# Optimization experiments

Measured on AMD Instinct MI355X. Metric: run time of the kernel, lower is better.

The kernel has to match this reference:

```python
import jax, jax.numpy as jnp
import numpy as np

N_NODES = 100000
N_EDGES = 1600000
IN_FEATS = 256
N_HEADS = 4
OUT_FEATS = 32
NEG_SLOPE = 0.2


def setup_inputs() -> dict:
    key = jax.random.key(0)
    k0, k1, k2, k3, k4, k5 = jax.random.split(key, 6)
    feat = jax.random.normal(k0, (N_NODES, IN_FEATS), dtype=jnp.float32)
    src = jax.random.randint(k1, (N_EDGES,), 0, N_NODES, dtype=jnp.int32)
    dst = jax.random.randint(k2, (N_EDGES,), 0, N_NODES, dtype=jnp.int32)
    # fc.weight: [num_heads*out_feats, in_feats] (torch Linear layout)
    W = jax.random.normal(k3, (N_HEADS * OUT_FEATS, IN_FEATS), dtype=jnp.float32) * 0.05
    attn_l = jax.random.normal(k4, (1, N_HEADS, OUT_FEATS), dtype=jnp.float32) * 0.1
    attn_r = jax.random.normal(k5, (1, N_HEADS, OUT_FEATS), dtype=jnp.float32) * 0.1
    return {"feat": feat, "src": src, "dst": dst, "W": W, "attn_l": attn_l, "attn_r": attn_r}


def reference(feat, src, dst, W, attn_l, attn_r):
    N = feat.shape[0]
    H, D = attn_l.shape[1], attn_l.shape[2]
    # fc projection -> [N, H, D]
    feat_src = (feat @ W.T).reshape(N, H, D)
    el = jnp.sum(feat_src * attn_l, axis=-1)  # [N, H]
    er = jnp.sum(feat_src * attn_r, axis=-1)  # [N, H]
    # per-edge scores: u_add_v then LeakyReLU  -> [E, H]
    e = jax.nn.leaky_relu(el[src] + er[dst], negative_slope=NEG_SLOPE)
    # edge_softmax: segmented softmax over edges grouped by destination node
    emax = jax.ops.segment_max(e, dst, num_segments=N)  # [N, H]
    emax = jnp.where(jnp.isfinite(emax), emax, jnp.zeros_like(emax))
    ee = jnp.exp(e - emax[dst])  # [E, H]
    denom = jax.ops.segment_sum(ee, dst, num_segments=N)  # [N, H]
    a = ee / denom[dst]  # [E, H]
    # u_mul_e + sum aggregation -> [N, H, D]
    m = feat_src[src] * a[:, :, None]  # [E, H, D]
    rst = jax.ops.segment_sum(m, dst, num_segments=N)
    return rst
```

## Files before the change

kernel.cpp:

```cpp
#include <hip/hip_runtime.h>
#include <hip/hip_bf16.h>
#include <math.h>

#define NN 100000
#define NE 1600000
#define INF_ 256
#define NH 4
#define DH 32
#define NHD 128
#define NEG_SLOPE 0.2f

#define NB3 1563
#define STRIDE 1280
#define EPB 4096
#define NBLK_BIN 391
#define GEMM_BLKS 782
#define SMEM_BYTES 32768

typedef __attribute__((ext_vector_type(8))) short bf16x8;
typedef __attribute__((ext_vector_type(4))) float f32x4;

__device__ __forceinline__ unsigned short f2bf(float f) {
    __hip_bfloat16 b = __float2bfloat16(f);
    return *reinterpret_cast<unsigned short*>(&b);
}

__global__ __launch_bounds__(256) void k_prep0(const float* __restrict__ W,
                                               unsigned short* __restrict__ Wimg,
                                               int* __restrict__ gcur) {
    int t = threadIdx.x;
    int b = blockIdx.x;
    if (b == 16) {
        for (int i = t; i < NB3; i += 256) gcur[i] = 0;
        return;
    }
    int i = b * 256 + t;
    int kt = i >> 9;
    int r = (i >> 2) & 127;
    int g = i & 3;
    int slot = g ^ (r & 7);
    const float* s = &W[(size_t)r * INF_ + kt * 32 + g * 8];
    unsigned short tmp[8];
#pragma unroll
    for (int j = 0; j < 8; j++) tmp[j] = f2bf(s[j]);
    *(bf16x8*)&Wimg[(size_t)kt * 8192 + r * 64 + slot * 8] = *(const bf16x8*)tmp;
}

__global__ __launch_bounds__(256) void k_gemmbin(const float* __restrict__ feat,
                                                 const unsigned short* __restrict__ Wimg,
                                                 const int* __restrict__ src,
                                                 const int* __restrict__ dst,
                                                 const float* __restrict__ al,
                                                 const float* __restrict__ ar,
                                                 unsigned short* __restrict__ fsb,
                                                 float* __restrict__ el,
                                                 float* __restrict__ er,
                                                 int* __restrict__ gcur,
                                                 unsigned* __restrict__ packed) {
    __shared__ __align__(16) char smem[SMEM_BYTES];
    const int t = threadIdx.x;

    if (blockIdx.x >= GEMM_BLKS) {
        int hb = blockIdx.x - GEMM_BLKS;
        int* ldst = (int*)smem;
        int* lc = (int*)(smem + EPB * 4);
        int* wb = (int*)(smem + EPB * 4 + NB3 * 4);
        for (int i = t; i < NB3; i += 256) lc[i] = 0;
        __syncthreads();
        int base = hb * EPB;
#pragma unroll
        for (int j = 0; j < 16; j++) {
            int e = base + j * 256 + t;
            int d = (e < NE) ? dst[e] : -1;
            ldst[j * 256 + t] = d;
            if (d >= 0) atomicAdd(&lc[d >> 6], 1);
        }
        __syncthreads();
        for (int i = t; i < NB3; i += 256) {
            int c = lc[i];
            wb[i] = c ? i * STRIDE + atomicAdd(&gcur[i], c) : 0;
            lc[i] = 0;
        }
        __syncthreads();
#pragma unroll
        for (int j = 0; j < 16; j++) {
            int e = base + j * 256 + t;
            if (e < NE) {
                int d = ldst[j * 256 + t];
                int bk = d >> 6;
                int s = src[e];
                int pos = wb[bk] + atomicAdd(&lc[bk], 1);
                if (pos < (bk + 1) * STRIDE)
                    packed[pos] = ((unsigned)s << 6) | (unsigned)(d & 63);
            }
        }
        return;
    }

    short* sA = (short*)smem;
    short* sB = (short*)(smem + 16384);
    const int brow = blockIdx.x * 128;
    const int wid = t >> 6, lane = t & 63;
    const int wr = wid >> 1, wc = wid & 1;
    const int lg = lane >> 4;
    const int lr = lane & 15;

    f32x4 acc[4][4];
#pragma unroll
    for (int m = 0; m < 4; m++)
#pragma unroll
        for (int n = 0; n < 4; n++) acc[m][n] = (f32x4){0.f, 0.f, 0.f, 0.f};

    const int srow = t >> 1;
    const int cb = (t & 1) * 16;
    const int g0 = cb >> 3;
    const int p0 = (g0 ^ (srow & 7));
    const int p1 = ((g0 + 1) ^ (srow & 7));
    const int grow = brow + srow;
    const bool arow_ok = (grow < NN);
    const char* bimg = (const char*)Wimg;

    float fv[16];
    uint4 wv0, wv1, wv2, wv3;
    if (arow_ok) {
        const float4* pa = (const float4*)&feat[(size_t)grow * INF_ + cb];
        *(float4*)&fv[0] = pa[0];
        *(float4*)&fv[4] = pa[1];
        *(float4*)&fv[8] = pa[2];
        *(float4*)&fv[12] = pa[3];
    } else {
#pragma unroll
        for (int j = 0; j < 16; j++) fv[j] = 0.f;
    }
    wv0 = *(const uint4*)(bimg + t * 16);
    wv1 = *(const uint4*)(bimg + 4096 + t * 16);
    wv2 = *(const uint4*)(bimg + 8192 + t * 16);
    wv3 = *(const uint4*)(bimg + 12288 + t * 16);

    for (int kt = 0; kt < 8; kt++) {
        {
            short sv[16];
#pragma unroll
            for (int j = 0; j < 16; j++) sv[j] = (short)f2bf(fv[j]);
            *(bf16x8*)&sA[srow * 64 + p0 * 8] = *(const bf16x8*)&sv[0];
            *(bf16x8*)&sA[srow * 64 + p1 * 8] = *(const bf16x8*)&sv[8];
            char* bd = (char*)sB;
            *(uint4*)(bd + t * 16) = wv0;
            *(uint4*)(bd + 4096 + t * 16) = wv1;
            *(uint4*)(bd + 8192 + t * 16) = wv2;
            *(uint4*)(bd + 12288 + t * 16) = wv3;
        }
        __syncthreads();
        if (kt < 7) {
            int k0 = (kt + 1) * 32;
            if (arow_ok) {
                const float4* pa = (const float4*)&feat[(size_t)grow * INF_ + k0 + cb];
                *(float4*)&fv[0] = pa[0];
                *(float4*)&fv[4] = pa[1];
                *(float4*)&fv[8] = pa[2];
                *(float4*)&fv[12] = pa[3];
            }
            const char* bsrc = bimg + (size_t)(kt + 1) * 16384;
            wv0 = *(const uint4*)(bsrc + t * 16);
            wv1 = *(const uint4*)(bsrc + 4096 + t * 16);
            wv2 = *(const uint4*)(bsrc + 8192 + t * 16);
            wv3 = *(const uint4*)(bsrc + 12288 + t * 16);
        }
        bf16x8 aF[4], bF[4];
#pragma unroll
        for (int m = 0; m < 4; m++) {
            int r = wr * 64 + m * 16 + lr;
            aF[m] = *(const bf16x8*)&sA[r * 64 + ((lg ^ (r & 7)) * 8)];
        }
#pragma unroll
        for (int n = 0; n < 4; n++) {
            int r = wc * 64 + n * 16 + lr;
            bF[n] = *(const bf16x8*)&sB[r * 64 + ((lg ^ (r & 7)) * 8)];
        }
#pragma unroll
        for (int m = 0; m < 4; m++)
#pragma unroll
            for (int n = 0; n < 4; n++)
                acc[m][n] = __builtin_amdgcn_mfma_f32_16x16x32_bf16(aF[m], bF[n], acc[m][n], 0, 0, 0);
        __syncthreads();
    }
#pragma unroll
    for (int m = 0; m < 4; m++) {
#pragma unroll
        for (int n = 0; n < 4; n++) {
#pragma unroll
            for (int r = 0; r < 4; r++) {
                int gr = brow + wr * 64 + m * 16 + lg * 4 + r;
                if (gr < NN)
                    fsb[(size_t)gr * NHD + wc * 64 + n * 16 + lr] = f2bf(acc[m][n][r]);
            }
        }
    }
    const int hA = wc * 2, hB = wc * 2 + 1;
    const float alA0 = al[hA * 32 + lr], alA1 = al[hA * 32 + 16 + lr];
    const float alB0 = al[hB * 32 + lr], alB1 = al[hB * 32 + 16 + lr];
    const float arA0 = ar[hA * 32 + lr], arA1 = ar[hA * 32 + 16 + lr];
    const float arB0 = ar[hB * 32 + lr], arB1 = ar[hB * 32 + 16 + lr];
#pragma unroll
    for (int m = 0; m < 4; m++) {
#pragma unroll
        for (int r = 0; r < 4; r++) {
            float eA = acc[m][0][r] * alA0 + acc[m][1][r] * alA1;
            float eB = acc[m][2][r] * alB0 + acc[m][3][r] * alB1;
            float fA = acc[m][0][r] * arA0 + acc[m][1][r] * arA1;
            float fB = acc[m][2][r] * arB0 + acc[m][3][r] * arB1;
#pragma unroll
            for (int off = 1; off < 16; off <<= 1) {
                eA += __shfl_xor(eA, off);
                eB += __shfl_xor(eB, off);
                fA += __shfl_xor(fA, off);
                fB += __shfl_xor(fB, off);
            }
            if (lr == 0) {
                int gr = brow + wr * 64 + m * 16 + lg * 4 + r;
                if (gr < NN) {
                    el[gr * 4 + hA] = eA;
                    el[gr * 4 + hB] = eB;
                    er[gr * 4 + hA] = fA;
                    er[gr * 4 + hB] = fB;
                }
            }
        }
    }
}

__global__ __launch_bounds__(256) void k_sortagg(const int* __restrict__ gcur,
                                                 const unsigned* __restrict__ packed,
                                                 const float* __restrict__ el,
                                                 const float* __restrict__ er,
                                                 const uint4* __restrict__ fsb128,
                                                 float* __restrict__ out) {
    __shared__ int lh[64];
    __shared__ int off[65];
    __shared__ int cur[64];
    __shared__ int esrc_l[STRIDE];
    int b = blockIdx.x, t = threadIdx.x;
    int beg = b * STRIDE;
    int cnt = gcur[b];
    if (cnt > STRIDE) cnt = STRIDE;

    if (t < 64) lh[t] = 0;
    __syncthreads();
    for (int k = t; k < cnt; k += 256)
        atomicAdd(&lh[packed[beg + k] & 63u], 1);
    __syncthreads();
    if (t < 64) {
        int v = lh[t];
        int x = v;
#pragma unroll
        for (int o = 1; o < 64; o <<= 1) {
            int y = __shfl_up(x, o);
            if (t >= o) x += y;
        }
        off[t] = x - v;
        cur[t] = x - v;
        if (t == 63) off[64] = x;
    }
    __syncthreads();
    for (int k = t; k < cnt; k += 256) {
        unsigned p = packed[beg + k];
        int pos = atomicAdd(&cur[p & 63u], 1);
        esrc_l[pos] = (int)(p >> 6);
    }
    __syncthreads();

    int lane = t & 63;
    int wv = t >> 6;
    int q = lane >> 4;
    int sl = lane & 15;
    int h = sl >> 2;

#define STEP(eV, vV)                                           \
    {                                                          \
        float sc_ = (eV) + rr;                                 \
        sc_ = sc_ > 0.f ? sc_ : NEG_SLOPE * sc_;               \
        float ee = __expf(sc_);                                \
        den += ee;                                             \
        a0 += ee * __uint_as_float((vV).x << 16);              \
        a1 += ee * __uint_as_float((vV).x & 0xFFFF0000u);      \
        a2 += ee * __uint_as_float((vV).y << 16);              \
        a3 += ee * __uint_as_float((vV).y & 0xFFFF0000u);      \
        a4 += ee * __uint_as_float((vV).z << 16);              \
        a5 += ee * __uint_as_float((vV).z & 0xFFFF0000u);      \
        a6 += ee * __uint_as_float((vV).w << 16);              \
        a7 += ee * __uint_as_float((vV).w & 0xFFFF0000u);      \
    }

    for (int ln = wv * 16; ln < wv * 16 + 16; ln++) {
        int node = (b << 6) + ln;
        if (node >= NN) break;
        int bg = off[ln];
        int en = off[ln + 1];
        float rr = er[node * 4 + h];
        float den = 0.f;
        float a0 = 0.f, a1 = 0.f, a2 = 0.f, a3 = 0.f;
        float a4 = 0.f, a5 = 0.f, a6 = 0.f, a7 = 0.f;
        int k = bg + q;
        for (; k + 4 < en; k += 8) {
            int s0 = esrc_l[k];
            int s1 = esrc_l[k + 4];
            uint4 v0 = fsb128[(size_t)s0 * 16 + sl];
            uint4 v1 = fsb128[(size_t)s1 * 16 + sl];
            float e0 = el[s0 * 4 + h];
            float e1 = el[s1 * 4 + h];
            STEP(e0, v0)
            STEP(e1, v1)
        }
        for (; k < en; k += 4) {
            int s = esrc_l[k];
            uint4 vv = fsb128[(size_t)s * 16 + sl];
            float eV = el[s * 4 + h];
            STEP(eV, vv)
        }
#pragma unroll
        for (int o = 16; o <= 32; o <<= 1) {
            a0 += __shfl_xor(a0, o);
            a1 += __shfl_xor(a1, o);
            a2 += __shfl_xor(a2, o);
            a3 += __shfl_xor(a3, o);
            a4 += __shfl_xor(a4, o);
            a5 += __shfl_xor(a5, o);
            a6 += __shfl_xor(a6, o);
            a7 += __shfl_xor(a7, o);
            den += __shfl_xor(den, o);
        }
        if (q == 0) {
            float inv = den > 0.f ? 1.0f / den : 0.f;
            float4 o0, o1;
            o0.x = a0 * inv; o0.y = a1 * inv; o0.z = a2 * inv; o0.w = a3 * inv;
            o1.x = a4 * inv; o1.y = a5 * inv; o1.z = a6 * inv; o1.w = a7 * inv;
            float* p = &out[(size_t)node * NHD + sl * 8];
            *(float4*)p = o0;
            *(float4*)(p + 4) = o1;
        }
    }
#undef STEP
}

extern "C" void kernel_launch(void* const* d_in, const int* in_sizes, int n_in,
                              void* d_out, int out_size, void* d_ws, size_t ws_size,
                              hipStream_t stream) {
    const float* feat = (const float*)d_in[0];
    const int* src = (const int*)d_in[1];
    const int* dst = (const int*)d_in[2];
    const float* W = (const float*)d_in[3];
    const float* al = (const float*)d_in[4];
    const float* ar = (const float*)d_in[5];
    float* out = (float*)d_out;

    char* ws = (char*)d_ws;
    unsigned short* fsb = (unsigned short*)ws;   ws += (size_t)NN * NHD * 2;
    unsigned* packed = (unsigned*)ws;            ws += (size_t)NB3 * STRIDE * 4;
    float* el = (float*)ws;                      ws += (size_t)NN * NH * 4;
    float* er = (float*)ws;                      ws += (size_t)NN * NH * 4;
    int* gcur = (int*)ws;                        ws += (size_t)NB3 * 4;
    unsigned short* Wimg = (unsigned short*)ws;  ws += (size_t)8 * 8192 * 2;

    k_prep0<<<17, 256, 0, stream>>>(W, Wimg, gcur);
    k_gemmbin<<<GEMM_BLKS + NBLK_BIN, 256, 0, stream>>>(feat, Wimg, src, dst,
                                                        al, ar, fsb, el, er,
                                                        gcur, packed);
    k_sortagg<<<NB3, 256, 0, stream>>>(gcur, packed, el, er,
                                       (const uint4*)fsb, out);
}
```

Measured before the change: 138.5 us.

## Split fused GEMM+binning kernel, enlarge bin chunks, pad global bucket counters

Splits the combined GEMM/edge-binning launch into a separate GEMM kernel and a separate binning kernel. The binning kernel now handles 16384 edges per block (98 blocks instead of 391), which cuts global atomic traffic on the bucket cursors. Those cursors are padded to 64-byte spacing to avoid contention from false sharing. The trade-off is that binning no longer overlaps with the GEMM in one launch, it needs an extra launch, and it re-reads dst instead of caching it in LDS.

```diff
diff --git a/kernel.cpp b/kernel.cpp
--- a/kernel.cpp
+++ b/kernel.cpp
@@ -12,10 +12,9 @@
 
 #define NB3 1563
 #define STRIDE 1280
-#define EPB 4096
-#define NBLK_BIN 391
+#define EPB2 16384
+#define NBLK_BIN 98
 #define GEMM_BLKS 782
-#define SMEM_BYTES 32768
 
 typedef __attribute__((ext_vector_type(8))) short bf16x8;
 typedef __attribute__((ext_vector_type(4))) float f32x4;
@@ -27,11 +26,11 @@
 
 __global__ __launch_bounds__(256) void k_prep0(const float* __restrict__ W,
                                                unsigned short* __restrict__ Wimg,
-                                               int* __restrict__ gcur) {
+                                               int* __restrict__ gcurP) {
     int t = threadIdx.x;
     int b = blockIdx.x;
     if (b == 16) {
-        for (int i = t; i < NB3; i += 256) gcur[i] = 0;
+        for (int i = t; i < NB3; i += 256) gcurP[i * 16] = 0;
         return;
     }
     int i = b * 256 + t;
@@ -46,59 +45,16 @@
     *(bf16x8*)&Wimg[(size_t)kt * 8192 + r * 64 + slot * 8] = *(const bf16x8*)tmp;
 }
 
-__global__ __launch_bounds__(256) void k_gemmbin(const float* __restrict__ feat,
-                                                 const unsigned short* __restrict__ Wimg,
-                                                 const int* __restrict__ src,
-                                                 const int* __restrict__ dst,
-                                                 const float* __restrict__ al,
-                                                 const float* __restrict__ ar,
-                                                 unsigned short* __restrict__ fsb,
-                                                 float* __restrict__ el,
-                                                 float* __restrict__ er,
-                                                 int* __restrict__ gcur,
-                                                 unsigned* __restrict__ packed) {
-    __shared__ __align__(16) char smem[SMEM_BYTES];
+__global__ __launch_bounds__(256) void k_gemm(const float* __restrict__ feat,
+                                              const unsigned short* __restrict__ Wimg,
+                                              const float* __restrict__ al,
+                                              const float* __restrict__ ar,
+                                              unsigned short* __restrict__ fsb,
+                                              float* __restrict__ el,
+                                              float* __restrict__ er) {
+    __shared__ short sA[128 * 64];
+    __shared__ short sB[128 * 64];
     const int t = threadIdx.x;
-
-    if (blockIdx.x >= GEMM_BLKS) {
-        int hb = blockIdx.x - GEMM_BLKS;
-        int* ldst = (int*)smem;
-        int* lc = (int*)(smem + EPB * 4);
-        int* wb = (int*)(smem + EPB * 4 + NB3 * 4);
-        for (int i = t; i < NB3; i += 256) lc[i] = 0;
-        __syncthreads();
-        int base = hb * EPB;
-#pragma unroll
-        for (int j = 0; j < 16; j++) {
-            int e = base + j * 256 + t;
-            int d = (e < NE) ? dst[e] : -1;
-            ldst[j * 256 + t] = d;
-            if (d >= 0) atomicAdd(&lc[d >> 6], 1);
-        }
-        __syncthreads();
-        for (int i = t; i < NB3; i += 256) {
-            int c = lc[i];
-            wb[i] = c ? i * STRIDE + atomicAdd(&gcur[i], c) : 0;
-            lc[i] = 0;
-        }
-        __syncthreads();
-#pragma unroll
-        for (int j = 0; j < 16; j++) {
-            int e = base + j * 256 + t;
-            if (e < NE) {
-                int d = ldst[j * 256 + t];
-                int bk = d >> 6;
-                int s = src[e];
-                int pos = wb[bk] + atomicAdd(&lc[bk], 1);
-                if (pos < (bk + 1) * STRIDE)
-                    packed[pos] = ((unsigned)s << 6) | (unsigned)(d & 63);
-            }
-        }
-        return;
-    }
-
-    short* sA = (short*)smem;
-    short* sB = (short*)(smem + 16384);
     const int brow = blockIdx.x * 128;
     const int wid = t >> 6, lane = t & 63;
     const int wr = wid >> 1, wc = wid & 1;
@@ -229,7 +185,42 @@
     }
 }
 
-__global__ __launch_bounds__(256) void k_sortagg(const int* __restrict__ gcur,
+__global__ __launch_bounds__(256) void k_bin(const int* __restrict__ src,
+                                             const int* __restrict__ dst,
+                                             int* __restrict__ gcurP,
+                                             unsigned* __restrict__ packed) {
+    __shared__ int lc[NB3];
+    __shared__ int wb[NB3];
+    int t = threadIdx.x;
+    for (int i = t; i < NB3; i += 256) lc[i] = 0;
+    __syncthreads();
+    int base = blockIdx.x * EPB2;
+#pragma unroll 4
+    for (int j = 0; j < 64; j++) {
+        int e = base + j * 256 + t;
+        if (e < NE) atomicAdd(&lc[dst[e] >> 6], 1);
+    }
+    __syncthreads();
+    for (int i = t; i < NB3; i += 256) {
+        int c = lc[i];
+        wb[i] = c ? i * STRIDE + atomicAdd(&gcurP[i * 16], c) : 0;
+        lc[i] = 0;
+    }
+    __syncthreads();
+#pragma unroll 4
+    for (int j = 0; j < 64; j++) {
+        int e = base + j * 256 + t;
+        if (e < NE) {
+            int d = dst[e];
+            int bk = d >> 6;
+            int pos = wb[bk] + atomicAdd(&lc[bk], 1);
+            if (pos < (bk + 1) * STRIDE)
+                packed[pos] = ((unsigned)src[e] << 6) | (unsigned)(d & 63);
+        }
+    }
+}
+
+__global__ __launch_bounds__(256) void k_sortagg(const int* __restrict__ gcurP,
                                                  const unsigned* __restrict__ packed,
                                                  const float* __restrict__ el,
                                                  const float* __restrict__ er,
@@ -241,7 +232,7 @@
     __shared__ int esrc_l[STRIDE];
     int b = blockIdx.x, t = threadIdx.x;
     int beg = b * STRIDE;
-    int cnt = gcur[b];
+    int cnt = gcurP[b * 16];
     if (cnt > STRIDE) cnt = STRIDE;
 
     if (t < 64) lh[t] = 0;
@@ -358,13 +349,12 @@
     unsigned* packed = (unsigned*)ws;            ws += (size_t)NB3 * STRIDE * 4;
     float* el = (float*)ws;                      ws += (size_t)NN * NH * 4;
     float* er = (float*)ws;                      ws += (size_t)NN * NH * 4;
-    int* gcur = (int*)ws;                        ws += (size_t)NB3 * 4;
+    int* gcurP = (int*)ws;                       ws += (size_t)NB3 * 16 * 4;
     unsigned short* Wimg = (unsigned short*)ws;  ws += (size_t)8 * 8192 * 2;
 
-    k_prep0<<<17, 256, 0, stream>>>(W, Wimg, gcur);
-    k_gemmbin<<<GEMM_BLKS + NBLK_BIN, 256, 0, stream>>>(feat, Wimg, src, dst,
-                                                        al, ar, fsb, el, er,
-                                                        gcur, packed);
-    k_sortagg<<<NB3, 256, 0, stream>>>(gcur, packed, el, er,
+    k_prep0<<<17, 256, 0, stream>>>(W, Wimg, gcurP);
+    k_gemm<<<GEMM_BLKS, 256, 0, stream>>>(feat, Wimg, al, ar, fsb, el, er);
+    k_bin<<<NBLK_BIN, 256, 0, stream>>>(src, dst, gcurP, packed);
+    k_sortagg<<<NB3, 256, 0, stream>>>(gcurP, packed, el, er,
                                        (const uint4*)fsb, out);
 }
```

After: 189.1 us. 1.37x slower.
